# Kernel optimization log

Measured on AMD Instinct MI355X. Metric: run time of the kernel, lower is better.

## Reference

```python
import jax, jax.numpy as jnp
import numpy as np
from jax import lax

BN_EPS = 1e-5


def _conv(x, w):
    # stride-1, VALID conv; the torch 'locally connected' layer shares weights
    # across pixels, so it is exactly a standard conv2d.
    return lax.conv_general_dilated(
        x, w, window_strides=(1, 1), padding='VALID',
        dimension_numbers=('NCHW', 'OIHW', 'NCHW'))


def _batchnorm(x, gamma, beta):
    # training-mode BatchNorm2d: batch statistics over (N, H, W)
    mean = jnp.mean(x, axis=(0, 2, 3), keepdims=True)
    var = jnp.var(x, axis=(0, 2, 3), keepdims=True)
    xhat = (x - mean) * lax.rsqrt(var + BN_EPS)
    return xhat * gamma[None, :, None, None] + beta[None, :, None, None]


def setup_inputs() -> dict:
    key = jax.random.key(0)
    ks = jax.random.split(key, 6)
    B = 16384
    x = jax.random.normal(ks[0], (B, 256), dtype=jnp.float32)
    w1 = jax.random.normal(ks[1], (16, 1, 3, 3), dtype=jnp.float32)
    w2 = jax.random.normal(ks[2], (32, 16, 2, 2), dtype=jnp.float32)
    w3 = jax.random.normal(ks[3], (64, 32, 1, 1), dtype=jnp.float32)
    fan_in = 64 * 13 * 13
    bound = 1.0 / np.sqrt(fan_in)
    fc_w = jax.random.uniform(ks[4], (10, fan_in), minval=-bound, maxval=bound, dtype=jnp.float32)
    fc_b = jax.random.uniform(ks[5], (10,), minval=-bound, maxval=bound, dtype=jnp.float32)
    return {
        'x': x, 'w1': w1, 'w2': w2, 'w3': w3,
        'g1': jnp.ones((16,), jnp.float32), 'b1': jnp.zeros((16,), jnp.float32),
        'g2': jnp.ones((32,), jnp.float32), 'b2': jnp.zeros((32,), jnp.float32),
        'g3': jnp.ones((64,), jnp.float32), 'b3': jnp.zeros((64,), jnp.float32),
        'fc_w': fc_w, 'fc_b': fc_b,
    }


def reference(x, w1, w2, w3, g1, b1, g2, b2, g3, b3, fc_w, fc_b):
    h = x.reshape(-1, 1, 16, 16)                     # [B,1,16,16]
    h = jax.nn.relu(_batchnorm(_conv(h, w1), g1, b1))  # [B,16,14,14]
    h = jax.nn.relu(_batchnorm(_conv(h, w2), g2, b2))  # [B,32,13,13]
    h = jax.nn.relu(_batchnorm(_conv(h, w3), g3, b3))  # [B,64,13,13]
    h = h.reshape(h.shape[0], -1)                    # [B, 64*13*13]
    # dropout is identity in eval/deterministic mode
    return h @ fc_w.T + fc_b                         # [B,10]
```

## Files before the change

### kernel.cpp

```cpp
#include <hip/hip_runtime.h>


#define NPART 1024
#define P2_OFF 32768
#define ST_OFF 229376
#define ST1 ST_OFF
#define ST2 (ST_OFF + 32)
#define ST3 (ST_OFF + 96)
#define C2R_OFF 230400
#define C1R_OFF 231424
#define C2P_OFF 262144
#define A2G_BYTE 5242880ull
#define FCB_N 86528
#define A1S 24
#define A1B 384

typedef __attribute__((ext_vector_type(8))) short bf16x8;
typedef __attribute__((ext_vector_type(4))) float f32x4;
typedef __attribute__((ext_vector_type(4))) unsigned int u32x4;

__device__ __forceinline__ unsigned int f2bf(float f) {
  unsigned int u = __float_as_uint(f);
  return (u + 0x7fffu + ((u >> 16) & 1u)) >> 16;
}
__device__ __forceinline__ unsigned int pkbf(float a, float b) {
  unsigned ua = __float_as_uint(a) + 0x8000u;
  unsigned ub = __float_as_uint(b) + 0x8000u;
  return __builtin_amdgcn_perm(ub, ua, 0x07060302u);
}
__device__ __forceinline__ bf16x8 mkfrag(uint2 a, uint2 b) {
  u32x4 u = {a.x, a.y, b.x, b.y};
  return __builtin_bit_cast(bf16x8, u);
}

__device__ __forceinline__ void conv1_mfma(
    const float* __restrict__ sxi,
    short* ph_buf,
    int r, int b, int q, bf16x8 a1f, f32x4 c1i)
{
  bf16x8 bf = {0, 0, 0, 0, 0, 0, 0, 0};
  unsigned* bu = (unsigned*)&bf;
  if (q == 0) {
    bu[0] = pkbf(sxi[r * 16 + b],           sxi[r * 16 + b + 1]);
    bu[1] = pkbf(sxi[r * 16 + b + 2],       sxi[(r + 1) * 16 + b]);
    bu[2] = pkbf(sxi[(r + 1) * 16 + b + 1], sxi[(r + 1) * 16 + b + 2]);
    bu[3] = pkbf(sxi[(r + 2) * 16 + b],     sxi[(r + 2) * 16 + b + 1]);
  } else if (q == 1) {
    bu[0] = pkbf(sxi[(r + 2) * 16 + b + 2], 0.f);
  }
  f32x4 acc = c1i;
  acc = __builtin_amdgcn_mfma_f32_16x16x32_bf16(a1f, bf, acc, 0, 0, 0);
  float v0 = acc[0] > 0.f ? acc[0] : 0.f;
  float v1 = acc[1] > 0.f ? acc[1] : 0.f;
  float v2 = acc[2] > 0.f ? acc[2] : 0.f;
  float v3 = acc[3] > 0.f ? acc[3] : 0.f;
  uint2 pk;
  pk.x = pkbf(v0, v1);
  pk.y = pkbf(v2, v3);
  *(uint2*)(ph_buf + (r & 1) * A1B + b * A1S + 4 * q) = pk;
}

__device__ __forceinline__ bf16x8 conv1_afrag(const float* w1, float rs1b,
                                              int b, int q) {
  bf16x8 v;
#pragma unroll
  for (int j = 0; j < 8; ++j) {
    int tap = 8 * q + j;
    v[j] = (tap < 9) ? (short)f2bf(w1[b * 9 + tap] * rs1b) : (short)0;
  }
  return v;
}

__global__ __launch_bounds__(256) void k1_xsyrk(
    const float* __restrict__ x, float* __restrict__ parts)
{
  __shared__ alignas(16) short sb[16 * 16 * 2 * 16];
  const int tid = threadIdx.x, w = tid >> 6, lane = tid & 63;
  const int b = lane & 15, q = lane >> 4;
  {
    const float4* xs = (const float4*)(x + (size_t)blockIdx.x * (16 * 256));
    for (int e = tid; e < 16 * 64; e += 256) {
      float4 v = xs[e];
      int img = e >> 6, row = (e >> 2) & 15, g = e & 3;
      uint2 pk;
      pk.x = pkbf(v.x, v.y);
      pk.y = pkbf(v.z, v.w);
      *(uint2*)(sb + ((img * 16 + row) * 2 + 0) * 16 + 4 * g) = pk;
    }
  }
  __syncthreads();
  {
    int img = tid >> 4, row = tid & 15;
    const unsigned* s0 = (const unsigned*)(sb + ((img * 16 + row) * 2 + 0) * 16);
    unsigned* s1 = (unsigned*)(sb + ((img * 16 + row) * 2 + 1) * 16);
    unsigned wprev = s0[0];
#pragma unroll
    for (int c = 0; c < 8; ++c) {
      unsigned wnext = (c < 7) ? s0[c + 1] : 0u;
      s1[c] = __builtin_amdgcn_perm(wnext, wprev, 0x05040302u);
      wprev = wnext;
    }
  }
  __syncthreads();
  const int di = (b < 9) ? (b / 3) : 0;
  const int dj = (b < 9) ? (b - di * 3) : 0;
  const int cp = dj & 1, dsh = dj >> 1;
  const int h = q >> 1, jb = (q & 1) * 8;
  const int wb = (jb >> 1) + dsh;
  f32x4 acc = {0.f, 0.f, 0.f, 0.f};
#pragma unroll 1
  for (int t = 0; t < 4; ++t) {
    const int ib = (w * 4 + t) * 16;
#pragma unroll 1
    for (int s = 0; s < 7; ++s) {
      bf16x8 af;
      unsigned* au = (unsigned*)&af;
      if (b < 9) {
        const unsigned* sr = (const unsigned*)(
            sb + ((ib + (2 * s + h + di)) * 2 + cp) * 16);
        au[0] = sr[wb];
        au[1] = sr[wb + 1];
        au[2] = sr[wb + 2];
        au[3] = (jb == 0) ? sr[wb + 3] : 0u;
      } else if (b == 9) {
#pragma unroll
        for (int cc = 0; cc < 4; ++cc) {
          unsigned lo = (jb + 2 * cc     < 14) ? 0x3F80u : 0u;
          unsigned hi = (jb + 2 * cc + 1 < 14) ? 0x3F800000u : 0u;
          au[cc] = lo | hi;
        }
      } else {
#pragma unroll
        for (int cc = 0; cc < 4; ++cc) au[cc] = 0u;
      }
      acc = __builtin_amdgcn_mfma_f32_16x16x32_bf16(af, af, acc, 0, 0, 0);
    }
  }
  __syncthreads();
  float* redc = (float*)sb;
#pragma unroll
  for (int rr = 0; rr < 4; ++rr)
    redc[w * 256 + (4 * q + rr) * 16 + b] = acc[rr];
  __syncthreads();
  parts[blockIdx.x * 256 + tid] =
      redc[tid] + redc[256 + tid] + redc[512 + tid] + redc[768 + tid];
}

__global__ __launch_bounds__(256) void k_stats1a(
    const float* __restrict__ parts, float* __restrict__ ws)
{
  const int e = blockIdx.x, tid = threadIdx.x;
  const int w = tid >> 6, lane = tid & 63;
  __shared__ float rs[4];
  float s = 0.f;
#pragma unroll 4
  for (int i = tid; i < 1024; i += 256) s += parts[i * 256 + e];
#pragma unroll
  for (int d = 1; d < 64; d <<= 1) s += __shfl_xor(s, d);
  if (lane == 0) rs[w] = s;
  __syncthreads();
  if (tid == 0) ws[C1R_OFF + e] = rs[0] + rs[1] + rs[2] + rs[3];
}

__global__ __launch_bounds__(64) void k_stats1b(
    const float* __restrict__ w1, const float* __restrict__ gamma,
    const float* __restrict__ beta, float* __restrict__ ws)
{
  const int c = threadIdx.x;
  if (c >= 16) return;
  const float* C = ws + C1R_OFF;
  float wr[9];
#pragma unroll
  for (int p = 0; p < 9; ++p) wr[p] = w1[c * 9 + p];
  float msum = 0.f;
#pragma unroll
  for (int p = 0; p < 9; ++p) msum += wr[p] * C[9 * 16 + p];
  float e2 = 0.f;
#pragma unroll
  for (int a = 0; a < 9; ++a)
#pragma unroll
    for (int bb = 0; bb < 9; ++bb)
      e2 += wr[a] * wr[bb] * C[a * 16 + bb];
  const float inv_n = 1.0f / (16384.0f * 196.0f);
  float mean = msum * inv_n;
  float var  = e2 * inv_n - mean * mean;
  float sv   = gamma[c] * rsqrtf(var + 1e-5f);
  ws[ST1 + c]      = sv;
  ws[ST1 + 16 + c] = beta[c] - mean * sv;
}

__global__ __launch_bounds__(256) void k_stats2(
    const float* __restrict__ gamma, const float* __restrict__ beta,
    float* __restrict__ ws, int nch, int part_off, int st_off, float inv_n)
{
  const int c = blockIdx.x, tid = threadIdx.x;
  const int w = tid >> 6, lane = tid & 63;
  __shared__ float rs[4], rq[4];
  float s = 0.f, q = 0.f;
#pragma unroll 4
  for (int i = tid; i < NPART; i += 256) {
    s += ws[part_off + i * 2 * nch + c];
    q += ws[part_off + i * 2 * nch + nch + c];
  }
#pragma unroll
  for (int d = 1; d < 64; d <<= 1) {
    s += __shfl_xor(s, d);
    q += __shfl_xor(q, d);
  }
  if (lane == 0) { rs[w] = s; rq[w] = q; }
  __syncthreads();
  if (tid == 0) {
    float st = rs[0] + rs[1] + rs[2] + rs[3];
    float qt = rq[0] + rq[1] + rq[2] + rq[3];
    float mean = st * inv_n;
    float var  = qt * inv_n - mean * mean;
    float sv   = gamma[c] * rsqrtf(var + 1e-5f);
    ws[st_off + c]       = sv;
    ws[st_off + nch + c] = beta[c] - mean * sv;
  }
}

__global__ __launch_bounds__(256) void k3_conv2_stats(
    const float* __restrict__ x, const float* __restrict__ w1,
    const float* __restrict__ w2, float* __restrict__ ws)
{
  __shared__ float sx_s[16 * 256 + 16];
  __shared__ alignas(16) short a1h[4 * 2 * A1B];
  __shared__ float redf[256];
  const int tid = threadIdx.x, w = tid >> 6, lane = tid & 63;
  const int b = lane & 15, q = lane >> 4;
  {
    const float4* xs = (const float4*)(x + (size_t)blockIdx.x * (16 * 256));
    float4* sd = (float4*)sx_s;
    for (int e = tid; e < 16 * 64; e += 256) sd[e] = xs[e];
    if (tid < 16) sx_s[16 * 256 + tid] = 0.f;
  }
  bf16x8 a1f = conv1_afrag(w1, ws[ST1 + b], b, q);
  f32x4 c1i;
#pragma unroll
  for (int r = 0; r < 4; ++r) c1i[r] = ws[ST1 + 16 + 4 * q + r];
  bf16x8 b2h[4];
#pragma unroll
  for (int ks = 0; ks < 2; ++ks)
#pragma unroll
    for (int nt = 0; nt < 2; ++nt) {
      bf16x8 vh;
#pragma unroll
      for (int j = 0; j < 8; ++j) {
        int kk = 8 * (q & 1) + j, dj = q >> 1;
        vh[j] = (short)f2bf(w2[(nt * 16 + b) * 64 + kk * 4 + ks * 2 + dj]);
      }
      b2h[ks * 2 + nt] = vh;
    }
  const float vb = (b < 13) ? 1.f : 0.f;
  const int colAr = (b + (q >> 1) < 15) ? (b + (q >> 1)) : 15;
  const int offAl = colAr * A1S + 8 * (q & 1);
  __syncthreads();

  float s2r[2][4] = {{0.f,0.f,0.f,0.f},{0.f,0.f,0.f,0.f}};
  float q2r[2][4] = {{0.f,0.f,0.f,0.f},{0.f,0.f,0.f,0.f}};
  short* ph = a1h + w * (2 * A1B);
#pragma unroll 1
  for (int t = 0; t < 4; ++t) {
    const float* sxi = sx_s + (w * 4 + t) * 256;
    conv1_mfma(sxi, ph, 0, b, q, a1f, c1i);
    __builtin_amdgcn_wave_barrier();
#pragma unroll 1
    for (int i = 0; i < 13; ++i) {
      conv1_mfma(sxi, ph, i + 1, b, q, a1f, c1i);
      __builtin_amdgcn_wave_barrier();
      bf16x8 ah0 = *(const bf16x8*)(ph + (i & 1) * A1B + offAl);
      bf16x8 ah1 = *(const bf16x8*)(ph + ((i + 1) & 1) * A1B + offAl);
      f32x4 acc2[2] = {{0.f,0.f,0.f,0.f},{0.f,0.f,0.f,0.f}};
#pragma unroll
      for (int nt = 0; nt < 2; ++nt) {
        acc2[nt] = __builtin_amdgcn_mfma_f32_16x16x32_bf16(b2h[nt], ah0, acc2[nt], 0, 0, 0);
        acc2[nt] = __builtin_amdgcn_mfma_f32_16x16x32_bf16(b2h[2 + nt], ah1, acc2[nt], 0, 0, 0);
      }
#pragma unroll
      for (int nt = 0; nt < 2; ++nt)
#pragma unroll
        for (int r = 0; r < 4; ++r) {
          float ym = acc2[nt][r] * vb;
          s2r[nt][r] += ym;
          q2r[nt][r] = fmaf(ym, acc2[nt][r], q2r[nt][r]);
        }
      __builtin_amdgcn_wave_barrier();
    }
  }
#pragma unroll
  for (int nt = 0; nt < 2; ++nt)
#pragma unroll
    for (int r = 0; r < 4; ++r) {
      float sv = s2r[nt][r], qv = q2r[nt][r];
      sv += __shfl_xor(sv, 1); sv += __shfl_xor(sv, 2);
      sv += __shfl_xor(sv, 4); sv += __shfl_xor(sv, 8);
      qv += __shfl_xor(qv, 1); qv += __shfl_xor(qv, 2);
      qv += __shfl_xor(qv, 4); qv += __shfl_xor(qv, 8);
      if (b == 0) {
        redf[w * 64 + nt * 16 + 4 * q + r]      = sv;
        redf[w * 64 + 32 + nt * 16 + 4 * q + r] = qv;
      }
    }
  __syncthreads();
  if (tid < 64)
    ws[P2_OFF + blockIdx.x * 64 + tid] =
        redf[tid] + redf[64 + tid] + redf[128 + tid] + redf[192 + tid];
}

__global__ __launch_bounds__(256) void k5_a2(
    const float* __restrict__ x, const float* __restrict__ w1,
    const float* __restrict__ w2, float* __restrict__ ws,
    short* __restrict__ a2g, float* __restrict__ parts)
{
  __shared__ float sx_s[16 * 256 + 16];
  __shared__ alignas(16) short a1h[4 * 2 * A1B];
  __shared__ alignas(16) short a2st[4 * 512];
  __shared__ float s2red[4 * 32];
  const int tid = threadIdx.x, w = tid >> 6, lane = tid & 63;
  const int b = lane & 15, q = lane >> 4;
  {
    const float4* xs = (const float4*)(x + (size_t)blockIdx.x * (16 * 256));
    float4* sd = (float4*)sx_s;
    for (int e = tid; e < 16 * 64; e += 256) sd[e] = xs[e];
    if (tid < 16) sx_s[16 * 256 + tid] = 0.f;
  }
  bf16x8 a1f = conv1_afrag(w1, ws[ST1 + b], b, q);
  f32x4 c1i;
#pragma unroll
  for (int r = 0; r < 4; ++r) c1i[r] = ws[ST1 + 16 + 4 * q + r];
  bf16x8 b2h[4];
#pragma unroll
  for (int ks = 0; ks < 2; ++ks)
#pragma unroll
    for (int nt = 0; nt < 2; ++nt) {
      float rs2b = ws[ST2 + nt * 16 + b];
      bf16x8 vh;
#pragma unroll
      for (int j = 0; j < 8; ++j) {
        int kk = 8 * (q & 1) + j, dj = q >> 1;
        vh[j] = (short)f2bf(w2[(nt * 16 + b) * 64 + kk * 4 + ks * 2 + dj] * rs2b);
      }
      b2h[ks * 2 + nt] = vh;
    }
  f32x4 c2i[2];
#pragma unroll
  for (int nt = 0; nt < 2; ++nt) {
    float t2b = ws[ST2 + 32 + nt * 16 + b];
#pragma unroll
    for (int r = 0; r < 4; ++r)
      c2i[nt][r] = (4 * q + r < 13) ? t2b : -1e30f;
  }
  const int colAr = (b + (q >> 1) < 15) ? (b + (q >> 1)) : 15;
  const int offAl = colAr * A1S + 8 * (q & 1);
  const u32x4 ou = {0x3F803F80u, 0x3F803F80u, 0x3F803F80u, 0x3F803F80u};
  const bf16x8 ones = __builtin_bit_cast(bf16x8, ou);
  __syncthreads();

  f32x4 accT0 = {0.f,0.f,0.f,0.f}, accT1 = {0.f,0.f,0.f,0.f},
        accT2 = {0.f,0.f,0.f,0.f};
  f32x4 accS0 = {0.f,0.f,0.f,0.f}, accS1 = {0.f,0.f,0.f,0.f};
  short* ph = a1h + w * (2 * A1B);
  short* st = a2st + w * 512;
#pragma unroll 1
  for (int t = 0; t < 4; ++t) {
    const int img = blockIdx.x * 16 + w * 4 + t;
    const float* sxi = sx_s + (w * 4 + t) * 256;
    short* gb = a2g + (size_t)img * 5408;
    conv1_mfma(sxi, ph, 0, b, q, a1f, c1i);
    __builtin_amdgcn_wave_barrier();
    uint2 pkp[2];
#pragma unroll 1
    for (int i = 0; i < 13; ++i) {
      conv1_mfma(sxi, ph, i + 1, b, q, a1f, c1i);
      __builtin_amdgcn_wave_barrier();
      bf16x8 ah0 = *(const bf16x8*)(ph + (i & 1) * A1B + offAl);
      bf16x8 ah1 = *(const bf16x8*)(ph + ((i + 1) & 1) * A1B + offAl);
      uint2 pkc[2];
#pragma unroll
      for (int nt = 0; nt < 2; ++nt) {
        f32x4 acc2 = c2i[nt];
        acc2 = __builtin_amdgcn_mfma_f32_16x16x32_bf16(ah0, b2h[nt], acc2, 0, 0, 0);
        acc2 = __builtin_amdgcn_mfma_f32_16x16x32_bf16(ah1, b2h[2 + nt], acc2, 0, 0, 0);
        float v0 = acc2[0] > 0.f ? acc2[0] : 0.f;
        float v1 = acc2[1] > 0.f ? acc2[1] : 0.f;
        float v2 = acc2[2] > 0.f ? acc2[2] : 0.f;
        float v3 = acc2[3] > 0.f ? acc2[3] : 0.f;
        uint2 pk;
        pk.x = pkbf(v0, v1);
        pk.y = pkbf(v2, v3);
        short* sp = st + nt * 16 + b;
        sp[(4 * q + 0) * 32] = (short)pk.x;
        sp[(4 * q + 1) * 32] = (short)(pk.x >> 16);
        sp[(4 * q + 2) * 32] = (short)pk.y;
        sp[(4 * q + 3) * 32] = (short)(pk.y >> 16);
        pkc[nt] = pk;
      }
      __builtin_amdgcn_wave_barrier();
      if (lane < 52) {
        bf16x8 vv = *(const bf16x8*)(st + lane * 8);
        *(bf16x8*)(gb + (size_t)i * 416 + lane * 8) = vv;
      }
      if (i & 1) {
        bf16x8 xf0 = mkfrag(pkp[0], pkc[0]);
        bf16x8 xf1 = mkfrag(pkp[1], pkc[1]);
        accT0 = __builtin_amdgcn_mfma_f32_16x16x32_bf16(xf0, xf0, accT0, 0, 0, 0);
        accT1 = __builtin_amdgcn_mfma_f32_16x16x32_bf16(xf0, xf1, accT1, 0, 0, 0);
        accT2 = __builtin_amdgcn_mfma_f32_16x16x32_bf16(xf1, xf1, accT2, 0, 0, 0);
        accS0 = __builtin_amdgcn_mfma_f32_16x16x32_bf16(ones, xf0, accS0, 0, 0, 0);
        accS1 = __builtin_amdgcn_mfma_f32_16x16x32_bf16(ones, xf1, accS1, 0, 0, 0);
      } else {
        pkp[0] = pkc[0];
        pkp[1] = pkc[1];
      }
      __builtin_amdgcn_wave_barrier();
    }
    {
      uint2 zz; zz.x = 0u; zz.y = 0u;
      bf16x8 xf0 = mkfrag(pkp[0], zz);
      bf16x8 xf1 = mkfrag(pkp[1], zz);
      accT0 = __builtin_amdgcn_mfma_f32_16x16x32_bf16(xf0, xf0, accT0, 0, 0, 0);
      accT1 = __builtin_amdgcn_mfma_f32_16x16x32_bf16(xf0, xf1, accT1, 0, 0, 0);
      accT2 = __builtin_amdgcn_mfma_f32_16x16x32_bf16(xf1, xf1, accT2, 0, 0, 0);
      accS0 = __builtin_amdgcn_mfma_f32_16x16x32_bf16(ones, xf0, accS0, 0, 0, 0);
      accS1 = __builtin_amdgcn_mfma_f32_16x16x32_bf16(ones, xf1, accS1, 0, 0, 0);
    }
  }
  if (q == 0) {
    s2red[w * 32 + b]      = accS0[0];
    s2red[w * 32 + 16 + b] = accS1[0];
  }
  float* redc = sx_s;
#pragma unroll
  for (int rr = 0; rr < 4; ++rr) {
    int m = 4 * q + rr;
    redc[w * 1024 + 0   + m * 16 + b] = accT0[rr];
    redc[w * 1024 + 256 + m * 16 + b] = accT1[rr];
    redc[w * 1024 + 512 + m * 16 + b] = accT2[rr];
  }
  __syncthreads();
  for (int e = tid; e < 768; e += 256)
    parts[blockIdx.x * 800 + e] =
        redc[e] + redc[1024 + e] + redc[2048 + e] + redc[3072 + e];
  if (tid < 32)
    parts[blockIdx.x * 800 + 768 + tid] =
        s2red[tid] + s2red[32 + tid] + s2red[64 + tid] + s2red[96 + tid];
}

__global__ __launch_bounds__(256) void k_statsC(
    const float* __restrict__ parts, float* __restrict__ ws)
{
  const int e = blockIdx.x, tid = threadIdx.x;
  const int w = tid >> 6, lane = tid & 63;
  __shared__ float rs[4];
  float s = 0.f;
#pragma unroll 4
  for (int i = tid; i < 1024; i += 256) s += parts[i * 800 + e];
#pragma unroll
  for (int d = 1; d < 64; d <<= 1) s += __shfl_xor(s, d);
  if (lane == 0) rs[w] = s;
  __syncthreads();
  if (tid == 0) ws[C2R_OFF + e] = rs[0] + rs[1] + rs[2] + rs[3];
}

__global__ __launch_bounds__(64) void k_stats3n(
    const float* __restrict__ w3, const float* __restrict__ gamma,
    const float* __restrict__ beta, float* __restrict__ ws)
{
  const int c3 = threadIdx.x;
  if (c3 >= 64) return;
  const float* C2R = ws + C2R_OFF;
  float wr[32];
#pragma unroll
  for (int k = 0; k < 32; ++k) wr[k] = w3[c3 * 32 + k];
  const float inv_n = 1.0f / (16384.0f * 169.0f);
  float msum = 0.f;
#pragma unroll
  for (int k = 0; k < 32; ++k) msum += wr[k] * C2R[768 + k];
  float e2 = 0.f;
  for (int a = 0; a < 16; ++a)
#pragma unroll
    for (int bb = 0; bb < 16; ++bb) {
      e2 += wr[a] * wr[bb] * C2R[a * 16 + bb];
      e2 += wr[16 + a] * wr[16 + bb] * C2R[512 + a * 16 + bb];
      e2 += 2.f * wr[a] * wr[16 + bb] * C2R[256 + a * 16 + bb];
    }
  float mean = msum * inv_n;
  float var  = e2 * inv_n - mean * mean;
  float sv   = gamma[c3] * rsqrtf(var + 1e-5f);
  ws[ST3 + c3]      = sv;
  ws[ST3 + 64 + c3] = beta[c3] - mean * sv;
}

__global__ __launch_bounds__(256) void k0_fcB(
    const float* __restrict__ fcw, unsigned int* __restrict__ fcB)
{
  int f = blockIdx.x * 256 + threadIdx.x;
  int u = f & 3, lane = (f >> 2) & 63, h = (f >> 8) & 1, p = f >> 9;
  int b = lane & 15, q = lane >> 4;
  unsigned lo = 0, hi = 0;
  if (b < 10) {
    int c30 = h * 32 + (u >> 1) * 16 + 4 * q + 2 * (u & 1);
    lo = f2bf(fcw[b * 10816 + c30 * 169 + p]);
    hi = f2bf(fcw[b * 10816 + (c30 + 1) * 169 + p]);
  }
  fcB[f] = lo | (hi << 16);
}

__global__ __launch_bounds__(256) void k7_fc(
    const short* __restrict__ a2g, const float* __restrict__ w3,
    const float* __restrict__ fcb, const float* __restrict__ ws,
    float* __restrict__ out)
{
  __shared__ float redf7[1024];
  const int tid = threadIdx.x, w = tid >> 6, lane = tid & 63;
  const int b = lane & 15, q = lane >> 4;
  bf16x8 b3h[4];
  f32x4 c3i[4];
#pragma unroll
  for (int nt = 0; nt < 4; ++nt) {
    float s3 = ws[ST3 + nt * 16 + b];
    bf16x8 vh;
#pragma unroll
    for (int j = 0; j < 8; ++j)
      vh[j] = (short)f2bf(w3[(nt * 16 + b) * 32 + 8 * q + j] * s3);
    b3h[nt] = vh;
#pragma unroll
    for (int r = 0; r < 4; ++r)
      c3i[nt][r] = ws[ST3 + 64 + nt * 16 + 4 * q + r];
  }
  const bf16x8* fcB = (const bf16x8*)ws;
  const short* abase = a2g + (size_t)(blockIdx.x * 16 + b) * 5408 + 8 * q;
  const int p0 = (w * 169) >> 2, p1 = ((w + 1) * 169) >> 2;
  f32x4 aF0 = {0.f, 0.f, 0.f, 0.f}, aF1 = {0.f, 0.f, 0.f, 0.f};
  bf16x8 vpre = *(const bf16x8*)(abase + p0 * 32);
  bf16x8 bw0 = fcB[(p0 * 2 + 0) * 64 + lane];
  bf16x8 bw1 = fcB[(p0 * 2 + 1) * 64 + lane];
#pragma unroll 1
  for (int p = p0; p < p1; ++p) {
    bf16x8 vc = vpre, f0 = bw0, f1 = bw1;
    if (p + 1 < p1) {
      vpre = *(const bf16x8*)(abase + (p + 1) * 32);
      bw0 = fcB[((p + 1) * 2 + 0) * 64 + lane];
      bw1 = fcB[((p + 1) * 2 + 1) * 64 + lane];
    }
    uint2 pkc[4];
#pragma unroll
    for (int nt = 0; nt < 4; ++nt) {
      f32x4 acc3 = c3i[nt];
      acc3 = __builtin_amdgcn_mfma_f32_16x16x32_bf16(b3h[nt], vc, acc3, 0, 0, 0);
      float v0 = acc3[0] > 0.f ? acc3[0] : 0.f;
      float v1 = acc3[1] > 0.f ? acc3[1] : 0.f;
      float v2 = acc3[2] > 0.f ? acc3[2] : 0.f;
      float v3 = acc3[3] > 0.f ? acc3[3] : 0.f;
      pkc[nt].x = pkbf(v0, v1);
      pkc[nt].y = pkbf(v2, v3);
    }
    aF0 = __builtin_amdgcn_mfma_f32_16x16x32_bf16(mkfrag(pkc[0], pkc[1]), f0, aF0, 0, 0, 0);
    aF1 = __builtin_amdgcn_mfma_f32_16x16x32_bf16(mkfrag(pkc[2], pkc[3]), f1, aF1, 0, 0, 0);
  }
#pragma unroll
  for (int r = 0; r < 4; ++r)
    redf7[w * 256 + (4 * q + r) * 16 + b] = aF0[r] + aF1[r];
  __syncthreads();
  if (tid < 160) {
    int img = tid / 10, jj = tid - img * 10;
    float s = redf7[img * 16 + jj] + redf7[256 + img * 16 + jj] +
              redf7[512 + img * 16 + jj] + redf7[768 + img * 16 + jj];
    out[(blockIdx.x * 16 + img) * 10 + jj] = s + fcb[jj];
  }
}

extern "C" void kernel_launch(void* const* d_in, const int* in_sizes, int n_in,
                              void* d_out, int out_size, void* d_ws, size_t ws_size,
                              hipStream_t stream) {
  (void)in_sizes; (void)n_in; (void)out_size; (void)ws_size;
  const float* x   = (const float*)d_in[0];
  const float* w1  = (const float*)d_in[1];
  const float* w2  = (const float*)d_in[2];
  const float* w3  = (const float*)d_in[3];
  const float* g1  = (const float*)d_in[4];
  const float* b1  = (const float*)d_in[5];
  const float* g2  = (const float*)d_in[6];
  const float* b2  = (const float*)d_in[7];
  const float* g3  = (const float*)d_in[8];
  const float* b3  = (const float*)d_in[9];
  const float* fcw = (const float*)d_in[10];
  const float* fcb = (const float*)d_in[11];
  float* out = (float*)d_out;
  float* ws  = (float*)d_ws;
  short* a2g = (short*)((char*)d_ws + A2G_BYTE);
  float* parts = ws + C2P_OFF;

  k1_xsyrk<<<1024, 256, 0, stream>>>(x, parts);
  k_stats1a<<<256, 256, 0, stream>>>(parts, ws);
  k_stats1b<<<1, 64, 0, stream>>>(w1, g1, b1, ws);
  k3_conv2_stats<<<1024, 256, 0, stream>>>(x, w1, w2, ws);
  k_stats2<<<32, 256, 0, stream>>>(g2, b2, ws, 32, P2_OFF, ST2,
                                   1.0f / (16384.0f * 169.0f));
  k5_a2<<<1024, 256, 0, stream>>>(x, w1, w2, ws, a2g, parts);
  k_statsC<<<800, 256, 0, stream>>>(parts, ws);
  k_stats3n<<<1, 64, 0, stream>>>(w3, g3, b3, ws);
  k0_fcB<<<FCB_N / 256, 256, 0, stream>>>(fcw, (unsigned int*)ws);
  k7_fc<<<1024, 256, 0, stream>>>(a2g, w3, fcb, ws, out);
}
```

Measured before the change: 254.9 us.

## Store raw conv2 output in stats pass; drop conv1/conv2 recompute in a2 kernel

The stats kernel k3 now also writes the raw bf16 conv2 pre-activations to global memory. The old k5 kernel recomputed conv1 and conv2 from x; the new k5_t instead reads those stored values back, applies the BN2 scale/shift and ReLU, rewrites them in place, and accumulates the Gram and sum statistics. This removes the duplicated conv1/conv2 MFMA work in exchange for an extra global write and read of the activation tensor, about 177 MB bf16 each way. Applying BN to bf16-rounded raw values, rather than folding the scale into the weights, slightly changes rounding.

```diff
diff --git a/kernel.cpp b/kernel.cpp
--- a/kernel.cpp
+++ b/kernel.cpp
@@ -14,6 +14,7 @@
 #define FCB_N 86528
 #define A1S 24
 #define A1B 384
+#define YSS 40
 
 typedef __attribute__((ext_vector_type(8))) short bf16x8;
 typedef __attribute__((ext_vector_type(4))) float f32x4;
@@ -222,10 +223,12 @@
 
 __global__ __launch_bounds__(256) void k3_conv2_stats(
     const float* __restrict__ x, const float* __restrict__ w1,
-    const float* __restrict__ w2, float* __restrict__ ws)
+    const float* __restrict__ w2, float* __restrict__ ws,
+    short* __restrict__ y2g)
 {
   __shared__ float sx_s[16 * 256 + 16];
   __shared__ alignas(16) short a1h[4 * 2 * A1B];
+  __shared__ alignas(16) short y2st[4 * 16 * YSS];
   __shared__ float redf[256];
   const int tid = threadIdx.x, w = tid >> 6, lane = tid & 63;
   const int b = lane & 15, q = lane >> 4;
@@ -260,9 +263,12 @@
   float s2r[2][4] = {{0.f,0.f,0.f,0.f},{0.f,0.f,0.f,0.f}};
   float q2r[2][4] = {{0.f,0.f,0.f,0.f},{0.f,0.f,0.f,0.f}};
   short* ph = a1h + w * (2 * A1B);
+  short* st = y2st + w * (16 * YSS);
 #pragma unroll 1
   for (int t = 0; t < 4; ++t) {
+    const int img = blockIdx.x * 16 + w * 4 + t;
     const float* sxi = sx_s + (w * 4 + t) * 256;
+    short* gb = y2g + (size_t)img * 5408;
     conv1_mfma(sxi, ph, 0, b, q, a1f, c1i);
     __builtin_amdgcn_wave_barrier();
 #pragma unroll 1
@@ -277,6 +283,15 @@
         acc2[nt] = __builtin_amdgcn_mfma_f32_16x16x32_bf16(b2h[nt], ah0, acc2[nt], 0, 0, 0);
         acc2[nt] = __builtin_amdgcn_mfma_f32_16x16x32_bf16(b2h[2 + nt], ah1, acc2[nt], 0, 0, 0);
       }
+      {
+        uint2 pz0, pz1;
+        pz0.x = pkbf(acc2[0][0], acc2[0][1]);
+        pz0.y = pkbf(acc2[0][2], acc2[0][3]);
+        pz1.x = pkbf(acc2[1][0], acc2[1][1]);
+        pz1.y = pkbf(acc2[1][2], acc2[1][3]);
+        *(uint2*)(st + b * YSS + 4 * q)      = pz0;
+        *(uint2*)(st + b * YSS + 16 + 4 * q) = pz1;
+      }
 #pragma unroll
       for (int nt = 0; nt < 2; ++nt)
 #pragma unroll
@@ -285,6 +300,11 @@
           s2r[nt][r] += ym;
           q2r[nt][r] = fmaf(ym, acc2[nt][r], q2r[nt][r]);
         }
+      __builtin_amdgcn_wave_barrier();
+      if (lane < 52) {
+        bf16x8 vv = *(const bf16x8*)(st + (lane >> 2) * YSS + (lane & 3) * 8);
+        *(bf16x8*)(gb + (size_t)i * 416 + lane * 8) = vv;
+      }
       __builtin_amdgcn_wave_barrier();
     }
   }
@@ -308,98 +328,80 @@
         redf[tid] + redf[64 + tid] + redf[128 + tid] + redf[192 + tid];
 }
 
-__global__ __launch_bounds__(256) void k5_a2(
-    const float* __restrict__ x, const float* __restrict__ w1,
-    const float* __restrict__ w2, float* __restrict__ ws,
-    short* __restrict__ a2g, float* __restrict__ parts)
-{
-  __shared__ float sx_s[16 * 256 + 16];
-  __shared__ alignas(16) short a1h[4 * 2 * A1B];
-  __shared__ alignas(16) short a2st[4 * 512];
+__global__ __launch_bounds__(256) void k5_t(
+    const float* __restrict__ ws, short* __restrict__ a2g,
+    float* __restrict__ parts)
+{
+  __shared__ float redc[4096];
+  __shared__ alignas(16) short st4[4 * 16 * YSS];
   __shared__ float s2red[4 * 32];
   const int tid = threadIdx.x, w = tid >> 6, lane = tid & 63;
   const int b = lane & 15, q = lane >> 4;
-  {
-    const float4* xs = (const float4*)(x + (size_t)blockIdx.x * (16 * 256));
-    float4* sd = (float4*)sx_s;
-    for (int e = tid; e < 16 * 64; e += 256) sd[e] = xs[e];
-    if (tid < 16) sx_s[16 * 256 + tid] = 0.f;
-  }
-  bf16x8 a1f = conv1_afrag(w1, ws[ST1 + b], b, q);
-  f32x4 c1i;
-#pragma unroll
-  for (int r = 0; r < 4; ++r) c1i[r] = ws[ST1 + 16 + 4 * q + r];
-  bf16x8 b2h[4];
-#pragma unroll
-  for (int ks = 0; ks < 2; ++ks)
-#pragma unroll
-    for (int nt = 0; nt < 2; ++nt) {
-      float rs2b = ws[ST2 + nt * 16 + b];
-      bf16x8 vh;
-#pragma unroll
-      for (int j = 0; j < 8; ++j) {
-        int kk = 8 * (q & 1) + j, dj = q >> 1;
-        vh[j] = (short)f2bf(w2[(nt * 16 + b) * 64 + kk * 4 + ks * 2 + dj] * rs2b);
-      }
-      b2h[ks * 2 + nt] = vh;
-    }
-  f32x4 c2i[2];
-#pragma unroll
-  for (int nt = 0; nt < 2; ++nt) {
-    float t2b = ws[ST2 + 32 + nt * 16 + b];
-#pragma unroll
-    for (int r = 0; r < 4; ++r)
-      c2i[nt][r] = (4 * q + r < 13) ? t2b : -1e30f;
-  }
-  const int colAr = (b + (q >> 1) < 15) ? (b + (q >> 1)) : 15;
-  const int offAl = colAr * A1S + 8 * (q & 1);
+  short* st = st4 + w * (16 * YSS);
+  if (lane < 15) {
+    u32x4 z = {0u, 0u, 0u, 0u};
+    *(bf16x8*)(st + 13 * YSS + lane * 8) = __builtin_bit_cast(bf16x8, z);
+  }
+  const int ch0 = (lane & 3) * 8;
+  f32x4 s2a = *(const f32x4*)(ws + ST2 + ch0);
+  f32x4 s2b = *(const f32x4*)(ws + ST2 + ch0 + 4);
+  f32x4 t2a = *(const f32x4*)(ws + ST2 + 32 + ch0);
+  f32x4 t2b = *(const f32x4*)(ws + ST2 + 32 + ch0 + 4);
   const u32x4 ou = {0x3F803F80u, 0x3F803F80u, 0x3F803F80u, 0x3F803F80u};
   const bf16x8 ones = __builtin_bit_cast(bf16x8, ou);
-  __syncthreads();
+  __builtin_amdgcn_wave_barrier();
 
   f32x4 accT0 = {0.f,0.f,0.f,0.f}, accT1 = {0.f,0.f,0.f,0.f},
         accT2 = {0.f,0.f,0.f,0.f};
   f32x4 accS0 = {0.f,0.f,0.f,0.f}, accS1 = {0.f,0.f,0.f,0.f};
-  short* ph = a1h + w * (2 * A1B);
-  short* st = a2st + w * 512;
 #pragma unroll 1
   for (int t = 0; t < 4; ++t) {
     const int img = blockIdx.x * 16 + w * 4 + t;
-    const float* sxi = sx_s + (w * 4 + t) * 256;
     short* gb = a2g + (size_t)img * 5408;
-    conv1_mfma(sxi, ph, 0, b, q, a1f, c1i);
-    __builtin_amdgcn_wave_barrier();
+    bf16x8 vv = {0, 0, 0, 0, 0, 0, 0, 0};
+    if (lane < 52) vv = *(const bf16x8*)(gb + lane * 8);
     uint2 pkp[2];
 #pragma unroll 1
     for (int i = 0; i < 13; ++i) {
-      conv1_mfma(sxi, ph, i + 1, b, q, a1f, c1i);
-      __builtin_amdgcn_wave_barrier();
-      bf16x8 ah0 = *(const bf16x8*)(ph + (i & 1) * A1B + offAl);
-      bf16x8 ah1 = *(const bf16x8*)(ph + ((i + 1) & 1) * A1B + offAl);
-      uint2 pkc[2];
-#pragma unroll
-      for (int nt = 0; nt < 2; ++nt) {
-        f32x4 acc2 = c2i[nt];
-        acc2 = __builtin_amdgcn_mfma_f32_16x16x32_bf16(ah0, b2h[nt], acc2, 0, 0, 0);
-        acc2 = __builtin_amdgcn_mfma_f32_16x16x32_bf16(ah1, b2h[2 + nt], acc2, 0, 0, 0);
-        float v0 = acc2[0] > 0.f ? acc2[0] : 0.f;
-        float v1 = acc2[1] > 0.f ? acc2[1] : 0.f;
-        float v2 = acc2[2] > 0.f ? acc2[2] : 0.f;
-        float v3 = acc2[3] > 0.f ? acc2[3] : 0.f;
-        uint2 pk;
-        pk.x = pkbf(v0, v1);
-        pk.y = pkbf(v2, v3);
-        short* sp = st + nt * 16 + b;
-        sp[(4 * q + 0) * 32] = (short)pk.x;
-        sp[(4 * q + 1) * 32] = (short)(pk.x >> 16);
-        sp[(4 * q + 2) * 32] = (short)pk.y;
-        sp[(4 * q + 3) * 32] = (short)(pk.y >> 16);
-        pkc[nt] = pk;
-      }
+      bf16x8 cur = vv;
+      if (i < 12 && lane < 52)
+        vv = *(const bf16x8*)(gb + (size_t)(i + 1) * 416 + lane * 8);
       __builtin_amdgcn_wave_barrier();
       if (lane < 52) {
-        bf16x8 vv = *(const bf16x8*)(st + lane * 8);
-        *(bf16x8*)(gb + (size_t)i * 416 + lane * 8) = vv;
+        float av[8];
+#pragma unroll
+        for (int j = 0; j < 4; ++j) {
+          float raw = __uint_as_float(
+              ((unsigned)(unsigned short)cur[j]) << 16);
+          float vj = fmaf(s2a[j], raw, t2a[j]);
+          av[j] = vj > 0.f ? vj : 0.f;
+        }
+#pragma unroll
+        for (int j = 0; j < 4; ++j) {
+          float raw = __uint_as_float(
+              ((unsigned)(unsigned short)cur[4 + j]) << 16);
+          float vj = fmaf(s2b[j], raw, t2b[j]);
+          av[4 + j] = vj > 0.f ? vj : 0.f;
+        }
+        u32x4 pq;
+        pq[0] = pkbf(av[0], av[1]);
+        pq[1] = pkbf(av[2], av[3]);
+        pq[2] = pkbf(av[4], av[5]);
+        pq[3] = pkbf(av[6], av[7]);
+        bf16x8 pv = __builtin_bit_cast(bf16x8, pq);
+        *(bf16x8*)(st + (lane >> 2) * YSS + (lane & 3) * 8) = pv;
+        *(bf16x8*)(gb + (size_t)i * 416 + lane * 8) = pv;
+      }
+      __builtin_amdgcn_wave_barrier();
+      uint2 pkc[2];
+#pragma unroll
+      for (int nt = 0; nt < 2; ++nt) {
+        unsigned r0 = (unsigned short)st[(4 * q + 0) * YSS + nt * 16 + b];
+        unsigned r1 = (unsigned short)st[(4 * q + 1) * YSS + nt * 16 + b];
+        unsigned r2 = (unsigned short)st[(4 * q + 2) * YSS + nt * 16 + b];
+        unsigned r3 = (unsigned short)st[(4 * q + 3) * YSS + nt * 16 + b];
+        pkc[nt].x = r0 | (r1 << 16);
+        pkc[nt].y = r2 | (r3 << 16);
       }
       if (i & 1) {
         bf16x8 xf0 = mkfrag(pkp[0], pkc[0]);
@@ -413,7 +415,6 @@
         pkp[0] = pkc[0];
         pkp[1] = pkc[1];
       }
-      __builtin_amdgcn_wave_barrier();
     }
     {
       uint2 zz; zz.x = 0u; zz.y = 0u;
@@ -430,7 +431,6 @@
     s2red[w * 32 + b]      = accS0[0];
     s2red[w * 32 + 16 + b] = accS1[0];
   }
-  float* redc = sx_s;
 #pragma unroll
   for (int rr = 0; rr < 4; ++rr) {
     int m = 4 * q + rr;
@@ -595,10 +595,10 @@
   k1_xsyrk<<<1024, 256, 0, stream>>>(x, parts);
   k_stats1a<<<256, 256, 0, stream>>>(parts, ws);
   k_stats1b<<<1, 64, 0, stream>>>(w1, g1, b1, ws);
-  k3_conv2_stats<<<1024, 256, 0, stream>>>(x, w1, w2, ws);
+  k3_conv2_stats<<<1024, 256, 0, stream>>>(x, w1, w2, ws, a2g);
   k_stats2<<<32, 256, 0, stream>>>(g2, b2, ws, 32, P2_OFF, ST2,
                                    1.0f / (16384.0f * 169.0f));
-  k5_a2<<<1024, 256, 0, stream>>>(x, w1, w2, ws, a2g, parts);
+  k5_t<<<1024, 256, 0, stream>>>(ws, a2g, parts);
   k_statsC<<<800, 256, 0, stream>>>(parts, ws);
   k_stats3n<<<1, 64, 0, stream>>>(w3, g3, b3, ws);
   k0_fcB<<<FCB_N / 256, 256, 0, stream>>>(fcw, (unsigned int*)ws);
```

Result: slower. 265.9 us (+4.3%).
